# Performance work log

Measured on AMD Instinct MI355X. Metric: run time of the kernel, lower is better.

The kernel has to match this reference:

```python
import jax, jax.numpy as jnp
import numpy as np

B, S, D_IN, D_OUT = 4, 2048, 768, 768

def setup_inputs() -> dict:
    key = jax.random.key(0)
    kx, kq, kk, kv = jax.random.split(key, 4)
    scale = 1.0 / np.sqrt(D_IN)
    return {
        "x": jax.random.normal(kx, (B, S, D_IN), dtype=jnp.float32),
        "Wq": jax.random.normal(kq, (D_OUT, D_IN), dtype=jnp.float32) * scale,
        "Wk": jax.random.normal(kk, (D_OUT, D_IN), dtype=jnp.float32) * scale,
        "Wv": jax.random.normal(kv, (D_OUT, D_IN), dtype=jnp.float32) * scale,
    }

def reference(x, Wq, Wk, Wv):
    # torch Linear: y = x @ W.T  (W is [d_out, d_in])
    q = jnp.einsum('bsd,od->bso', x, Wq)
    k = jnp.einsum('bsd,od->bso', x, Wk)
    v = jnp.einsum('bsd,od->bso', x, Wv)
    scores = jnp.einsum('bqo,bko->bqk', q, k)  # [B,S,S]
    causal = jnp.tril(jnp.ones((scores.shape[1], scores.shape[2]), dtype=bool))
    neg_inf = jnp.array(-jnp.inf, dtype=scores.dtype)
    scores = jnp.where(causal, scores, neg_inf)
    inv_sqrt_d = jnp.asarray(1.0 / np.sqrt(q.shape[-1]), dtype=scores.dtype)
    weights = jax.nn.softmax(scores * inv_sqrt_d, axis=-1)
    # dropout p=0.0 -> identity
    return jnp.einsum('bqk,bko->bqo', weights, v)
```

## Files before the change

kernel.cpp:

```cpp
#include <hip/hip_runtime.h>
#include <hip/hip_bf16.h>
#include <cstdint>
#include <cstddef>


typedef __attribute__((ext_vector_type(8))) short short8;
typedef __attribute__((ext_vector_type(4))) float f32x4;

#define GPTR(p) (const __attribute__((address_space(1))) void*)(p)
#define LPTR(p) (__attribute__((address_space(3))) void*)(p)
#define MFMA16(a8, b8, c) c = __builtin_amdgcn_mfma_f32_16x16x32_bf16(a8, b8, c, 0, 0, 0)

constexpr int CB = 4, CS = 2048, CD = 768;
constexpr int CBS = CB * CS;

typedef const __attribute__((address_space(3))) char* lds_cp;

__device__ __forceinline__ short8 ds_read128(const __hip_bfloat16* p) {
    short8 r;
    lds_cp a = (lds_cp)p;
    asm volatile("ds_read_b128 %0, %1" : "=v"(r) : "v"(a));
    return r;
}

__device__ __forceinline__ int xcd_swz(int bid, int nwg) {
    return (bid & 7) * (nwg >> 3) + (bid >> 3);
}

__device__ inline unsigned short f2bf_bits(float v) {
    __hip_bfloat16 h = __float2bfloat16(v);
    unsigned short u;
    __builtin_memcpy(&u, &h, 2);
    return u;
}

__device__ inline ushort4 cvt4(float4 f) {
    ushort4 u;
    u.x = f2bf_bits(f.x); u.y = f2bf_bits(f.y);
    u.z = f2bf_bits(f.z); u.w = f2bf_bits(f.w);
    return u;
}

template <int MI>
__device__ __forceinline__ void zero_acc(f32x4 (&acc)[MI][4]) {
#pragma unroll
    for (int i = 0; i < MI; ++i)
#pragma unroll
        for (int j = 0; j < 4; ++j)
            acc[i][j] = f32x4{0.f, 0.f, 0.f, 0.f};
}

__global__ __launch_bounds__(256) void cvt_all(
    const float4* __restrict__ x,  const float4* __restrict__ wq,
    const float4* __restrict__ wk, const float4* __restrict__ wv,
    ushort4* __restrict__ x16, ushort4* __restrict__ w16,
    float4* __restrict__ rsum4)
{
    constexpr int NX = CBS * CD / 4;
    constexpr int NW = CD * CD / 4;
    constexpr int NT = NX + 3 * NW;
    const int i = blockIdx.x * 256 + threadIdx.x;
    if (i < NX) {
        x16[i] = cvt4(x[i]);
    } else if (i < NT) {
        const int j = i - NX;
        if (j < NW)            w16[j] = cvt4(wq[j]);
        else if (j < 2 * NW)   w16[j] = cvt4(wk[j - NW]);
        else                   w16[j] = cvt4(wv[j - 2 * NW]);
    } else {
        const int j = i - NT;
        rsum4[j] = float4{0.f, 0.f, 0.f, 0.f};
    }
}

__device__ __forceinline__ void gemm256_core(
    const __hip_bfloat16* __restrict__ A,
    const __hip_bfloat16* __restrict__ B,
    __hip_bfloat16* As, __hip_bfloat16* Bs,
    int m0, int n0, int K, int nkt,
    f32x4 (&acc)[8][4])
{
    const int t   = threadIdx.x;
    const int w   = t >> 6;
    const int l   = t & 63;
    const int lq  = l >> 4;
    const int lm  = l & 15;
    const int wm  = w >> 2;
    const int wn  = w & 3;
    const int lm7 = lm & 7;
    const int c0  = (lq ^ lm7) << 3;
    const int c1  = c0 ^ 32;

    const int rr0   = t >> 3;
    const int gp8   = (t & 7) << 3;
    const int g8    = (((t & 7) ^ (rr0 & 7)) << 3);
    const int rowBa = ((rr0 & 32) << 1) | (rr0 & 31);

    const __hip_bfloat16* Aori = A + (size_t)m0 * K;
    const __hip_bfloat16* Bori = B + (size_t)n0 * K;

    auto stage = [&](int reg, int bufT, int kt) {
        const int kc = kt * 64 + g8;
        const __hip_bfloat16* s0;
        __hip_bfloat16* d;
        if (reg == 0) {
            s0 = Aori + (size_t)rr0 * K + kc;
            d  = As + bufT * 16384 + rr0 * 64 + gp8;
        } else if (reg == 2) {
            s0 = Aori + (size_t)(64 + rr0) * K + kc;
            d  = As + bufT * 16384 + (64 + rr0) * 64 + gp8;
        } else if (reg == 3) {
            s0 = Bori + (size_t)rowBa * K + kc;
            d  = Bs + bufT * 16384 + rowBa * 64 + gp8;
        } else {
            s0 = Bori + (size_t)(32 + rowBa) * K + kc;
            d  = Bs + bufT * 16384 + (32 + rowBa) * 64 + gp8;
        }
        __builtin_amdgcn_global_load_lds(GPTR(s0), LPTR(d), 16, 0, 0);
        __builtin_amdgcn_global_load_lds(GPTR(s0 + (size_t)128 * K), LPTR(d + 8192), 16, 0, 0);
    };

    stage(0, 0, 0); stage(1, 0, 0); stage(2, 0, 0); stage(3, 0, 0);
    stage(0, 1, 1); stage(1, 1, 1); stage(2, 1, 1);
    asm volatile("s_waitcnt vmcnt(6)" ::: "memory");
    __builtin_amdgcn_s_barrier();

    for (int kt = 0; kt < nkt; ++kt) {
        const int buf = kt & 1;
        const __hip_bfloat16* Ab = As + buf * 16384 + wm * 8192 + lm * 64;
        const __hip_bfloat16* Bb = Bs + buf * 16384 + (wn >> 1) * 8192 + (wn & 1) * 4096 + lm * 64;
        short8 alo[4][2], ahi[4][2], ba[2][2], bb[2][2];

#pragma unroll
        for (int i = 0; i < 4; ++i) {
            alo[i][0] = ds_read128(&Ab[i * 1024 + c0]);
            alo[i][1] = ds_read128(&Ab[i * 1024 + c1]);
        }
#pragma unroll
        for (int j = 0; j < 2; ++j) {
            ba[j][0] = ds_read128(&Bb[j * 1024 + c0]);
            ba[j][1] = ds_read128(&Bb[j * 1024 + c1]);
        }
#pragma unroll
        for (int j = 0; j < 2; ++j) {
            bb[j][0] = ds_read128(&Bb[(2 + j) * 1024 + c0]);
            bb[j][1] = ds_read128(&Bb[(2 + j) * 1024 + c1]);
        }

        if (kt + 1 < nkt) stage(3, buf ^ 1, kt + 1);
        __builtin_amdgcn_s_barrier();
        asm volatile("s_waitcnt lgkmcnt(4)");
        __builtin_amdgcn_sched_barrier(0);
        __builtin_amdgcn_s_setprio(1);
#pragma unroll
        for (int i = 0; i < 4; ++i)
#pragma unroll
            for (int j = 0; j < 2; ++j) {
                MFMA16(alo[i][0], ba[j][0], acc[i][j]);
                MFMA16(alo[i][1], ba[j][1], acc[i][j]);
            }
        __builtin_amdgcn_s_setprio(0);
        __builtin_amdgcn_s_barrier();

        if (kt + 2 < nkt) stage(0, buf, kt + 2);
        __builtin_amdgcn_s_barrier();
        asm volatile("s_waitcnt lgkmcnt(0)");
        __builtin_amdgcn_sched_barrier(0);
        __builtin_amdgcn_s_setprio(1);
#pragma unroll
        for (int i = 0; i < 4; ++i)
#pragma unroll
            for (int j = 0; j < 2; ++j) {
                MFMA16(alo[i][0], bb[j][0], acc[i][2 + j]);
                MFMA16(alo[i][1], bb[j][1], acc[i][2 + j]);
            }
        __builtin_amdgcn_s_setprio(0);
        __builtin_amdgcn_s_barrier();

#pragma unroll
        for (int i = 0; i < 4; ++i) {
            ahi[i][0] = ds_read128(&Ab[(4 + i) * 1024 + c0]);
            ahi[i][1] = ds_read128(&Ab[(4 + i) * 1024 + c1]);
        }
        if (kt + 2 < nkt) stage(1, buf, kt + 2);
        __builtin_amdgcn_s_barrier();
        asm volatile("s_waitcnt lgkmcnt(0)");
        __builtin_amdgcn_sched_barrier(0);
        __builtin_amdgcn_s_setprio(1);
#pragma unroll
        for (int i = 0; i < 4; ++i)
#pragma unroll
            for (int j = 0; j < 2; ++j) {
                MFMA16(ahi[i][0], bb[j][0], acc[4 + i][2 + j]);
                MFMA16(ahi[i][1], bb[j][1], acc[4 + i][2 + j]);
            }
        __builtin_amdgcn_s_setprio(0);
        __builtin_amdgcn_s_barrier();

        if (kt + 2 < nkt) stage(2, buf, kt + 2);
        __builtin_amdgcn_s_setprio(1);
#pragma unroll
        for (int i = 0; i < 4; ++i)
#pragma unroll
            for (int j = 0; j < 2; ++j) {
                MFMA16(ahi[i][0], ba[j][0], acc[4 + i][j]);
                MFMA16(ahi[i][1], ba[j][1], acc[4 + i][j]);
            }
        __builtin_amdgcn_s_setprio(0);
        if (kt + 2 < nkt) {
            asm volatile("s_waitcnt vmcnt(6)" ::: "memory");
        } else if (kt + 1 < nkt) {
            asm volatile("s_waitcnt vmcnt(0)" ::: "memory");
        }
        __builtin_amdgcn_s_barrier();
    }
}

__global__ __launch_bounds__(512, 2) void scores_vt_gemm(
    const __hip_bfloat16* __restrict__ q16,
    const __hip_bfloat16* __restrict__ k16,
    const __hip_bfloat16* __restrict__ x16,
    const __hip_bfloat16* __restrict__ w16,
    __hip_bfloat16* __restrict__ sp16,
    __hip_bfloat16* __restrict__ vt16,
    float* __restrict__ rowsum,
    float scale)
{
    __shared__ __align__(16) __hip_bfloat16 As[2 * 16384];
    __shared__ __align__(16) __hip_bfloat16 Bs[2 * 16384];

    const int id = xcd_swz(blockIdx.x, 240);
    const __hip_bfloat16 *A, *B;
    int m0, n0, b;
    const bool is_sc = (id < 144);
    if (is_sc) {
        b = id / 36;
        const int tt = id % 36;
        int mi = (int)((sqrtf(8.f * tt + 1.f) - 1.f) * 0.5f);
        while ((mi + 1) * (mi + 2) / 2 <= tt) ++mi;
        while (mi * (mi + 1) / 2 > tt) --mi;
        const int nj = tt - mi * (mi + 1) / 2;
        m0 = mi * 256; n0 = nj * 256;
        A = q16 + (size_t)b * CS * CD;
        B = k16 + (size_t)b * CS * CD;
    } else {
        int r = id - 144;
        b = r / 24; r %= 24;
        m0 = (r >> 3) * 256;
        n0 = (r & 7) * 256;
        A = w16 + (size_t)2 * CD * CD;
        B = x16 + (size_t)b * CS * CD;
    }

    f32x4 acc[8][4];
    zero_acc<8>(acc);
    gemm256_core(A, B, As, Bs, m0, n0, CD, CD / 64, acc);

    const int t = threadIdx.x, w = t >> 6, l = t & 63, lq = l >> 4, lm = l & 15;
    const int wm = w >> 2, wn = w & 3;

    if (is_sc) {
        __hip_bfloat16* C = sp16 + (size_t)b * CS * CS;
        float* rs = rowsum + (size_t)b * CS;
#pragma unroll
        for (int i = 0; i < 8; ++i) {
            float psum[4] = {0.f, 0.f, 0.f, 0.f};
#pragma unroll
            for (int j = 0; j < 4; ++j) {
                const int n = n0 + wn * 64 + j * 16 + lm;
#pragma unroll
                for (int r2 = 0; r2 < 4; ++r2) {
                    const int m = m0 + wm * 128 + i * 16 + lq * 4 + r2;
                    float e = (n <= m) ? __expf(acc[i][j][r2] * scale) : 0.f;
                    C[(size_t)m * CS + n] = __float2bfloat16(e);
                    psum[r2] += e;
                }
            }
#pragma unroll
            for (int r2 = 0; r2 < 4; ++r2) {
#pragma unroll
                for (int off = 1; off < 16; off <<= 1)
                    psum[r2] += __shfl_xor(psum[r2], off);
                if (lm == 0) {
                    const int m = m0 + wm * 128 + i * 16 + lq * 4 + r2;
                    atomicAdd(&rs[m], psum[r2]);
                }
            }
        }
    } else {
        __hip_bfloat16* C = vt16 + (size_t)b * CD * CS;
#pragma unroll
        for (int i = 0; i < 8; ++i)
#pragma unroll
            for (int j = 0; j < 4; ++j) {
                const int n = n0 + wn * 64 + j * 16 + lm;
#pragma unroll
                for (int r2 = 0; r2 < 4; ++r2) {
                    const int m = m0 + wm * 128 + i * 16 + lq * 4 + r2;
                    C[(size_t)m * CS + n] = __float2bfloat16(acc[i][j][r2]);
                }
            }
    }
}

template <int BM>
__device__ __forceinline__ void gemm_core(
    const __hip_bfloat16* __restrict__ A,
    const __hip_bfloat16* __restrict__ B,
    __hip_bfloat16* As, __hip_bfloat16* Bs,
    int m0, int n0, int K, int kend,
    f32x4 (&acc)[BM / 32][4])
{
    constexpr int AC = BM / 16;
    constexpr int SC = AC + 8;
    constexpr int MI = BM / 32;

    const int t  = threadIdx.x;
    const int w  = t >> 6;
    const int l  = t & 63;
    const int lq = l >> 4;
    const int lm = l & 15;
    const int wm = (w >> 1) * (BM / 2);
    const int wn = (w & 1) * 64;

    const int srow = l >> 2;
    const int scol = (l & 3) * 8;

    auto stage = [&](int buf, int k0) {
#pragma unroll
        for (int ci = 0; ci < SC / 4; ++ci) {
            const int c = ci * 4 + w;
            if (c < AC) {
                __builtin_amdgcn_global_load_lds(
                    GPTR(A + (size_t)(m0 + c * 16 + srow) * K + k0 + scol),
                    LPTR(&As[buf * BM * 32 + c * 512]), 16, 0, 0);
            } else {
                const int c2 = c - AC;
                __builtin_amdgcn_global_load_lds(
                    GPTR(B + (size_t)(n0 + c2 * 16 + srow) * K + k0 + scol),
                    LPTR(&Bs[buf * 128 * 32 + c2 * 512]), 16, 0, 0);
            }
        }
    };

    stage(0, 0);
    asm volatile("s_waitcnt vmcnt(0)" ::: "memory");
    __syncthreads();

    int cur = 0;
    for (int k0 = 0; k0 < kend; k0 += 32) {
        if (k0 + 32 < kend)
            stage(cur ^ 1, k0 + 32);

        short8 af[MI], bf[4];
#pragma unroll
        for (int i = 0; i < MI; ++i)
            af[i] = *(const short8*)&As[cur * BM * 32 + (wm + i * 16 + lm) * 32 + lq * 8];
#pragma unroll
        for (int j = 0; j < 4; ++j)
            bf[j] = *(const short8*)&Bs[cur * 128 * 32 + (wn + j * 16 + lm) * 32 + lq * 8];

#pragma unroll
        for (int i = 0; i < MI; ++i)
#pragma unroll
            for (int j = 0; j < 4; ++j)
                acc[i][j] = __builtin_amdgcn_mfma_f32_16x16x32_bf16(
                    af[i], bf[j], acc[i][j], 0, 0, 0);

        __syncthreads();
        cur ^= 1;
    }
}

__global__ __launch_bounds__(256) void qk_gemm(
    const __hip_bfloat16* __restrict__ x16,
    const __hip_bfloat16* __restrict__ w16,
    __hip_bfloat16* __restrict__ q16,
    __hip_bfloat16* __restrict__ k16)
{
    __shared__ __align__(16) __hip_bfloat16 As[2 * 128 * 32];
    __shared__ __align__(16) __hip_bfloat16 Bs[2 * 128 * 32];

    const int id   = xcd_swz(blockIdx.x, 768);
    const int proj = id / 384;
    const int r    = id % 384;
    const int n0   = (r % 6) * 128;
    const int m0   = (r / 6) * 128;

    f32x4 acc[4][4];
    zero_acc<4>(acc);
    gemm_core<128>(x16, w16 + (size_t)proj * CD * CD, As, Bs, m0, n0, CD, CD, acc);

    __hip_bfloat16* C = proj ? k16 : q16;
    const int t  = threadIdx.x;
    const int w  = t >> 6;
    const int l  = t & 63;
    const int lq = l >> 4;
    const int lm = l & 15;
    const int wm = (w >> 1) * 64;
    const int wn = (w & 1) * 64;
#pragma unroll
    for (int i = 0; i < 4; ++i)
#pragma unroll
        for (int j = 0; j < 4; ++j) {
            const int n = n0 + wn + j * 16 + lm;
#pragma unroll
            for (int r2 = 0; r2 < 4; ++r2) {
                const int m = m0 + wm + i * 16 + lq * 4 + r2;
                C[(size_t)m * CD + n] = __float2bfloat16(acc[i][j][r2]);
            }
        }
}

__global__ __launch_bounds__(256) void pv_gemm(
    const __hip_bfloat16* __restrict__ sp16,
    const __hip_bfloat16* __restrict__ vt16,
    const float* __restrict__ rowsum,
    float* __restrict__ out)
{
    const int id   = xcd_swz(blockIdx.x, 768);
    const int mrev = id / 24;
    int r          = id % 24;
    const int b    = r / 6;
    const int n0   = (r % 6) * 128;
    const int mi   = 31 - mrev;
    const int m0   = mi * 64;
    const int kend = m0 + 64;

    __shared__ __align__(16) __hip_bfloat16 As[2 * 64 * 32];
    __shared__ __align__(16) __hip_bfloat16 Bs[2 * 128 * 32];

    const __hip_bfloat16* A = sp16 + (size_t)b * CS * CS;
    const __hip_bfloat16* B = vt16 + (size_t)b * CD * CS;
    float* Co = out + (size_t)b * CS * CD;
    const float* rs = rowsum + (size_t)b * CS;

    f32x4 acc[2][4];
    zero_acc<2>(acc);
    gemm_core<64>(A, B, As, Bs, m0, n0, CS, kend, acc);

    const int t  = threadIdx.x;
    const int w  = t >> 6;
    const int l  = t & 63;
    const int lq = l >> 4;
    const int lm = l & 15;
    const int wm = (w >> 1) * 32;
    const int wn = (w & 1) * 64;

#pragma unroll
    for (int i = 0; i < 2; ++i) {
        float inv[4];
#pragma unroll
        for (int r2 = 0; r2 < 4; ++r2)
            inv[r2] = 1.0f / rs[m0 + wm + i * 16 + lq * 4 + r2];
#pragma unroll
        for (int j = 0; j < 4; ++j) {
            const int n = n0 + wn + j * 16 + lm;
#pragma unroll
            for (int r2 = 0; r2 < 4; ++r2) {
                const int m = m0 + wm + i * 16 + lq * 4 + r2;
                Co[(size_t)m * CD + n] = acc[i][j][r2] * inv[r2];
            }
        }
    }
}

extern "C" void kernel_launch(void* const* d_in, const int* in_sizes, int n_in,
                              void* d_out, int out_size, void* d_ws, size_t ws_size,
                              hipStream_t stream)
{
    const float* x  = (const float*)d_in[0];
    const float* Wq = (const float*)d_in[1];
    const float* Wk = (const float*)d_in[2];
    const float* Wv = (const float*)d_in[3];
    float* out = (float*)d_out;

    char* ws = (char*)d_ws;
    size_t off = 0;
    auto alloc = [&](size_t bytes) { char* p = ws + off; off += bytes; return p; };

    __hip_bfloat16* x16  = (__hip_bfloat16*)alloc((size_t)CBS * CD * 2);
    __hip_bfloat16* q16  = (__hip_bfloat16*)alloc((size_t)CBS * CD * 2);
    __hip_bfloat16* k16  = (__hip_bfloat16*)alloc((size_t)CBS * CD * 2);
    __hip_bfloat16* vt16 = (__hip_bfloat16*)alloc((size_t)CBS * CD * 2);
    __hip_bfloat16* sp16 = (__hip_bfloat16*)alloc((size_t)CB * CS * CS * 2);
    __hip_bfloat16* w16  = (__hip_bfloat16*)alloc((size_t)3 * CD * CD * 2);
    float*          rsum = (float*)alloc((size_t)CB * CS * sizeof(float));

    constexpr int NCVT_BLK = (CBS * CD + 3 * CD * CD) / 4 / 256 + 8;
    cvt_all<<<NCVT_BLK, 256, 0, stream>>>(
        (const float4*)x, (const float4*)Wq, (const float4*)Wk, (const float4*)Wv,
        (ushort4*)x16, (ushort4*)w16, (float4*)rsum);

    qk_gemm<<<768, 256, 0, stream>>>(x16, w16, q16, k16);

    scores_vt_gemm<<<240, 512, 0, stream>>>(
        q16, k16, x16, w16, sp16, vt16, rsum, 0.03608439182435161f);

    pv_gemm<<<768, 256, 0, stream>>>(sp16, vt16, rsum, out);
}
```

Baseline: 186.5 us.

## Add double-buffered 64-wide K-step pv_core with direct global-to-LDS loads

Replaces the generic gemm_core in the P·V GEMM with a dedicated core that stages 64-wide K slabs into double-buffered LDS using global_load_lds. The next tile is prefetched while MFMAs run on the current one, with one barrier per 64-wide K step. It also drops the XCD block swizzle and uses blockIdx.x directly, which may hurt L2 locality across chiplets. LDS use grows to 48 KB per block, which may lower occupancy.

```diff
diff --git a/kernel.cpp b/kernel.cpp
--- a/kernel.cpp
+++ b/kernel.cpp
@@ -412,13 +412,85 @@
         }
 }
 
+__device__ __forceinline__ void pv_core(
+    const __hip_bfloat16* __restrict__ A,
+    const __hip_bfloat16* __restrict__ B,
+    __hip_bfloat16* As, __hip_bfloat16* Bs,
+    int m0, int n0, int K, int kend,
+    f32x4 (&acc)[2][4])
+{
+    constexpr int AC = 4;
+    constexpr int SC = AC + 8;
+
+    const int t  = threadIdx.x;
+    const int w  = t >> 6;
+    const int l  = t & 63;
+    const int lq = l >> 4;
+    const int lm = l & 15;
+    const int wm = (w >> 1) * 32;
+    const int wn = (w & 1) * 64;
+
+    const int srow = l >> 2;
+    const int scol = (l & 3) * 8;
+
+    auto stage = [&](int buf, int k0) {
+#pragma unroll
+        for (int ci = 0; ci < 2 * SC / 4; ++ci) {
+            const int c    = ci * 4 + w;
+            const int slab = (c >= SC) ? 1 : 0;
+            const int cc   = c - slab * SC;
+            const int kofs = k0 + slab * 32 + scol;
+            if (cc < AC) {
+                __builtin_amdgcn_global_load_lds(
+                    GPTR(A + (size_t)(m0 + cc * 16 + srow) * K + kofs),
+                    LPTR(&As[buf * 4096 + slab * 2048 + cc * 512]), 16, 0, 0);
+            } else {
+                const int c2 = cc - AC;
+                __builtin_amdgcn_global_load_lds(
+                    GPTR(B + (size_t)(n0 + c2 * 16 + srow) * K + kofs),
+                    LPTR(&Bs[buf * 8192 + slab * 4096 + c2 * 512]), 16, 0, 0);
+            }
+        }
+    };
+
+    stage(0, 0);
+    asm volatile("s_waitcnt vmcnt(0)" ::: "memory");
+    __syncthreads();
+
+    int cur = 0;
+    for (int k0 = 0; k0 < kend; k0 += 64) {
+        if (k0 + 64 < kend)
+            stage(cur ^ 1, k0 + 64);
+
+#pragma unroll
+        for (int kk = 0; kk < 2; ++kk) {
+            short8 af[2], bf[4];
+#pragma unroll
+            for (int i = 0; i < 2; ++i)
+                af[i] = *(const short8*)&As[cur * 4096 + kk * 2048 + (wm + i * 16 + lm) * 32 + lq * 8];
+#pragma unroll
+            for (int j = 0; j < 4; ++j)
+                bf[j] = *(const short8*)&Bs[cur * 8192 + kk * 4096 + (wn + j * 16 + lm) * 32 + lq * 8];
+#pragma unroll
+            for (int i = 0; i < 2; ++i)
+#pragma unroll
+                for (int j = 0; j < 4; ++j)
+                    acc[i][j] = __builtin_amdgcn_mfma_f32_16x16x32_bf16(
+                        af[i], bf[j], acc[i][j], 0, 0, 0);
+        }
+
+        __syncthreads();
+        cur ^= 1;
+    }
+}
+
 __global__ __launch_bounds__(256) void pv_gemm(
     const __hip_bfloat16* __restrict__ sp16,
     const __hip_bfloat16* __restrict__ vt16,
     const float* __restrict__ rowsum,
     float* __restrict__ out)
 {
-    const int id   = xcd_swz(blockIdx.x, 768);
+    const int id   = blockIdx.x;
     const int mrev = id / 24;
     int r          = id % 24;
     const int b    = r / 6;
@@ -427,8 +499,8 @@
     const int m0   = mi * 64;
     const int kend = m0 + 64;
 
-    __shared__ __align__(16) __hip_bfloat16 As[2 * 64 * 32];
-    __shared__ __align__(16) __hip_bfloat16 Bs[2 * 128 * 32];
+    __shared__ __align__(16) __hip_bfloat16 As[2 * 4096];
+    __shared__ __align__(16) __hip_bfloat16 Bs[2 * 8192];
 
     const __hip_bfloat16* A = sp16 + (size_t)b * CS * CS;
     const __hip_bfloat16* B = vt16 + (size_t)b * CD * CS;
@@ -437,7 +509,7 @@
 
     f32x4 acc[2][4];
     zero_acc<2>(acc);
-    gemm_core<64>(A, B, As, Bs, m0, n0, CS, kend, acc);
+    pv_core(A, B, As, Bs, m0, n0, CS, kend, acc);
 
     const int t  = threadIdx.x;
     const int w  = t >> 6;
```

Measured after the change: 174.7 us. -6.3%, faster.
